# Performance work log

Hardware: AMD Instinct MI355X
Metric: run time of the kernel (lower is better)

## Reference

```python
import jax, jax.numpy as jnp
import numpy as np

WINDOW = 25          # window_size -> h = w = 25, n = 625 tokens
DIM = 512
DIM_HEAD = 64
HEADS = DIM // DIM_HEAD
BATCH = 64


def _rel_pos_indices(ws):
    # mirrors the torch buffer: pairwise relative offsets on a ws x ws grid
    pos = np.arange(ws)
    gi, gj = np.meshgrid(pos, pos, indexing='ij')
    grid = np.stack([gi.reshape(-1), gj.reshape(-1)], axis=-1)      # (ws*ws, 2)
    rel = grid[:, None, :] - grid[None, :, :] + (ws - 1)            # (n, n, 2)
    return (rel[..., 0] * (2 * ws - 1) + rel[..., 1]).astype(np.int32)


def setup_inputs() -> dict:
    key = jax.random.key(0)
    k1, k2, k3, k4 = jax.random.split(key, 4)
    x = jax.random.normal(k1, (BATCH, DIM, WINDOW, WINDOW), jnp.float32)
    w_qkv = jax.random.normal(k2, (DIM, 3 * DIM), jnp.float32) * 0.02   # to_qkv weight (x @ w_qkv)
    w_out = jax.random.normal(k3, (DIM, DIM), jnp.float32) * 0.02       # to_out weight
    rel_pos_bias = jax.random.normal(k4, ((2 * WINDOW - 1) ** 2, HEADS), jnp.float32) * 0.02
    rel_pos_indices = jnp.asarray(_rel_pos_indices(WINDOW))
    return {"x": x, "w_qkv": w_qkv, "w_out": w_out,
            "rel_pos_bias": rel_pos_bias, "rel_pos_indices": rel_pos_indices}


def reference(x, w_qkv, w_out, rel_pos_bias, rel_pos_indices):
    b, d, h, w = x.shape
    n = h * w
    dh = DIM_HEAD
    m = d // dh
    scale = dh ** -0.5
    tokens = x.reshape(b, d, n).transpose(0, 2, 1)                  # b n d
    qkv = tokens @ w_qkv                                            # b n 3d
    q, k, v = jnp.split(qkv, 3, axis=-1)
    split_heads = lambda t: t.reshape(b, n, m, dh).transpose(0, 2, 1, 3)  # b m n dh
    q = split_heads(q) * scale
    k = split_heads(k)
    v = split_heads(v)
    sim = jnp.einsum('bmid,bmjd->bmij', q, k)                       # b m n n
    bias = rel_pos_bias[rel_pos_indices]                            # n n m  (embedding lookup)
    sim = sim + bias.transpose(2, 0, 1)[None]                       # add rel-pos bias inline
    attn = jax.nn.softmax(sim, axis=-1)
    out = jnp.einsum('bmij,bmjd->bmid', attn, v)                    # b m n dh
    out = out.transpose(0, 2, 1, 3).reshape(b, n, m * dh)           # concat heads
    out = out @ w_out                                               # b n d
    return out.transpose(0, 2, 1).reshape(b, d, h, w)
```

## Files before the change

kernel.cpp:

```cpp
#include <hip/hip_runtime.h>
#include <cstdint>
#include <cstddef>

typedef unsigned short u16;
typedef __attribute__((ext_vector_type(8))) short bf16x8;
typedef __attribute__((ext_vector_type(4))) float f32x4;

#define NB    64
#define NTOK  625
#define NTOKP 640
#define DDIM  512
#define NH    8
#define DH    64

__device__ __forceinline__ float bf2f(u16 v) {
    return __uint_as_float(((unsigned int)v) << 16);
}
__device__ __forceinline__ u16 f2bf(float f) {
    unsigned int x = __float_as_uint(f);
    unsigned int r = (x + 0x7fffu + ((x >> 16) & 1u)) >> 16;
    return (u16)r;
}
__device__ __forceinline__ u16 f2bf_fast(float f) {
    return (u16)((__float_as_uint(f) + 0x8000u) >> 16);
}

#if __has_builtin(__builtin_amdgcn_global_load_lds)
#define HAVE_GLDS 1
typedef const __attribute__((address_space(1))) void gas_void;
typedef __attribute__((address_space(3))) void las_void;
__device__ __forceinline__ void glds16(const void* g, void* l) {
    __builtin_amdgcn_global_load_lds((gas_void*)g, (las_void*)l, 16, 0, 0);
}
#else
#define HAVE_GLDS 0
__device__ __forceinline__ void glds16(const void* g, void* l) {
    *(uint4*)l = *(const uint4*)g;
}
#endif

__global__ __launch_bounds__(256) void k_transpose_x(const float* __restrict__ x,
                                                     u16* __restrict__ tokens) {
    __shared__ u16 T[64][66];
    int b = blockIdx.z, ct = blockIdx.y, it = blockIdx.x;
    int t = threadIdx.x;
    int i0 = it * 64, c0 = ct * 64;
#pragma unroll
    for (int r = 0; r < 2; r++) {
        int c = (t >> 3) + r * 32;
        int i8 = (t & 7) * 8;
        const float* s = x + ((size_t)b * DDIM + c0 + c) * NTOK + i0 + i8;
#pragma unroll
        for (int u = 0; u < 8; u++)
            T[c][i8 + u] = (i0 + i8 + u < NTOK) ? f2bf(s[u]) : (u16)0;
    }
    __syncthreads();
#pragma unroll
    for (int r = 0; r < 2; r++) {
        int i = (t >> 3) + r * 32;
        int c8 = (t & 7) * 8;
        int gi = i0 + i;
        if (gi < NTOK) {
            u16* d = tokens + ((size_t)b * NTOK + gi) * DDIM + c0 + c8;
#pragma unroll
            for (int u = 0; u < 8; u++) d[u] = T[c8 + u][i];
        }
    }
}

__global__ __launch_bounds__(256) void k_transpose_w(const float* __restrict__ src,
                                                     u16* __restrict__ dst, int R, int C) {
    __shared__ u16 T[64][66];
    int r0 = blockIdx.y * 64, c0 = blockIdx.x * 64;
    int t = threadIdx.x;
#pragma unroll
    for (int rr = 0; rr < 2; rr++) {
        int r = (t >> 3) + rr * 32;
        int c8 = (t & 7) * 8;
        const float* s = src + (size_t)(r0 + r) * C + c0 + c8;
#pragma unroll
        for (int u = 0; u < 8; u++) T[r][c8 + u] = f2bf(s[u]);
    }
    __syncthreads();
#pragma unroll
    for (int rr = 0; rr < 2; rr++) {
        int c = (t >> 3) + rr * 32;
        int r8 = (t & 7) * 8;
        u16* d = dst + (size_t)(c0 + c) * R + r0 + r8;
#pragma unroll
        for (int u = 0; u < 8; u++) d[u] = T[r8 + u][c];
    }
}

__global__ __launch_bounds__(256) void k_bias(const int* __restrict__ rpi,
                                              const float* __restrict__ rpb,
                                              u16* __restrict__ biasC) {
    int blk = blockIdx.x;
    int m = blk / 100, jt = (blk / 10) % 10, it = blk % 10;
    int t = threadIdx.x;
    u16 vals[16];
#pragma unroll
    for (int jj = 0; jj < 4; jj++) {
        int gj = jt * 64 + jj * 16 + (t & 15);
#pragma unroll
        for (int r = 0; r < 4; r++) {
            int gi = it * 64 + (t >> 6) * 16 + ((t >> 4) & 3) * 4 + r;
            float v;
            if (gj >= NTOK) v = -1e30f;
            else if (gi >= NTOK) v = 0.f;
            else v = rpb[rpi[gi * NTOK + gj] * NH + m];
            vals[jj * 4 + r] = f2bf(v);
        }
    }
    u16* d = biasC + ((size_t)(m * 10 + jt) * 10 + it) * 4096 + t * 16;
    *(uint4*)d = *(uint4*)&vals[0];
    *(uint4*)(d + 8) = *(uint4*)&vals[8];
}

__global__ __launch_bounds__(256) void k_qkv(const u16* __restrict__ tokens,
                                             const u16* __restrict__ wT,
                                             u16* __restrict__ qk, u16* __restrict__ vT) {
    __shared__ u16 SMEM[9216];
    int b = blockIdx.z, jt = blockIdx.y, it = blockIdx.x;
    int i0 = it * 128, j0 = jt * 128;
    int t = threadIdx.x;
    int w = t >> 6, lane = t & 63, quad = lane >> 4, l15 = lane & 15;
    int wr = w >> 1, wc = w & 1;
    f32x4 acc[4][4] = {};
    const u16* abase = tokens + ((size_t)b * NTOK + i0) * DDIM;
    const u16* bbase = wT + (size_t)j0 * DDIM;
    for (int k0 = 0; k0 < DDIM; k0 += 32) {
        __syncthreads();
#pragma unroll
        for (int c = 0; c < 2; c++) {
            int unit = c * 256 + t;
            int row = unit >> 2, col = (unit & 3) * 8;
            glds16(abase + (size_t)row * DDIM + k0 + col, SMEM + unit * 8);
            glds16(bbase + (size_t)row * DDIM + k0 + col, SMEM + 4096 + unit * 8);
        }
        __syncthreads();
        bf16x8 af[4], bfv[4];
#pragma unroll
        for (int q2 = 0; q2 < 4; q2++) {
            af[q2]  = *(const bf16x8*)&SMEM[(wr * 64 + q2 * 16 + l15) * 32 + quad * 8];
            bfv[q2] = *(const bf16x8*)&SMEM[4096 + (wc * 64 + q2 * 16 + l15) * 32 + quad * 8];
        }
#pragma unroll
        for (int ii = 0; ii < 4; ii++)
#pragma unroll
            for (int jj = 0; jj < 4; jj++)
                acc[ii][jj] = __builtin_amdgcn_mfma_f32_16x16x32_bf16(af[ii], bfv[jj], acc[ii][jj], 0, 0, 0);
    }
    __syncthreads();
    if (jt < 8) {
        float scale = (j0 < 512) ? 0.125f : 1.0f;
#pragma unroll
        for (int h = 0; h < 2; h++) {
            if (h) __syncthreads();
            if (wr == h) {
#pragma unroll
                for (int ii = 0; ii < 4; ii++)
#pragma unroll
                    for (int jj = 0; jj < 4; jj++)
#pragma unroll
                        for (int r = 0; r < 4; r++)
                            SMEM[(ii * 16 + quad * 4 + r) * 136 + wc * 64 + jj * 16 + l15] =
                                f2bf(acc[ii][jj][r] * scale);
            }
            __syncthreads();
#pragma unroll
            for (int g = 0; g < 4; g++) {
                int unit = g * 256 + t;
                int tok = unit >> 4, ch8 = (unit & 15) * 8;
                int gi = i0 + h * 64 + tok;
                if (gi < NTOK)
                    *(uint4*)(qk + ((size_t)b * NTOK + gi) * 1024 + j0 + ch8) =
                        *(uint4*)&SMEM[tok * 136 + ch8];
            }
        }
    } else {
        int ch0 = j0 - 1024;
#pragma unroll
        for (int h = 0; h < 2; h++) {
            if (h) __syncthreads();
            if (wr == h) {
#pragma unroll
                for (int ii = 0; ii < 4; ii++)
#pragma unroll
                    for (int jj = 0; jj < 4; jj++)
#pragma unroll
                        for (int r = 0; r < 4; r++) {
                            int tok = ii * 16 + quad * 4 + r;
                            int gi = i0 + h * 64 + tok;
                            u16 val = (gi < NTOK) ? f2bf(acc[ii][jj][r]) : (u16)0;
                            SMEM[(wc * 64 + jj * 16 + l15) * 72 + (tok & 15) * 4 + (tok >> 4)] = val;
                        }
            }
            __syncthreads();
#pragma unroll
            for (int g = 0; g < 4; g++) {
                int unit = g * 256 + t;
                int chl = unit >> 3, tok8 = (unit & 7) * 8;
                int chv = ch0 + chl, hd = chv >> 6, tc = chv & 63;
                *(uint4*)(vT + (((size_t)b * NH + hd) * DH + tc) * NTOKP + i0 + h * 64 + tok8) =
                    *(uint4*)&SMEM[chl * 72 + tok8];
            }
        }
    }
}

__global__ __launch_bounds__(256) void k_attn(const u16* __restrict__ qk,
                                              const u16* __restrict__ vT,
                                              const u16* __restrict__ biasC,
                                              u16* __restrict__ attnout) {
    __shared__ u16 Qs[64][72];
    __shared__ u16 Ks[64][72];
    __shared__ u16 Vs[64][72];
    __shared__ u16 Ps[64][72];
    int b = blockIdx.z, m = blockIdx.y, it = blockIdx.x;
    int i0 = it * 64;
    int t = threadIdx.x;
    int w = t >> 6, lane = t & 63, quad = lane >> 4, l15 = lane & 15;
#pragma unroll
    for (int r = 0; r < 2; r++) {
        int row = (t >> 3) + r * 32;
        int t8 = (t & 7) * 8;
        int gi = i0 + row;
        uint4 v;
        if (gi < NTOK) v = *(const uint4*)(qk + ((size_t)b * NTOK + gi) * 1024 + m * DH + t8);
        else v = make_uint4(0, 0, 0, 0);
        *(uint4*)&Qs[row][t8] = v;
    }
    float rs[4] = {0.f, 0.f, 0.f, 0.f};
    f32x4 oacc[4] = {};
    const u16* vbase = vT + ((size_t)b * NH + m) * DH * NTOKP;
    const u16* bC = biasC + (size_t)(m * 10) * 10 * 4096 + (size_t)it * 4096 + t * 16;

    for (int jt = 0; jt < 10; jt++) {
        int j0 = jt * 64;
        __syncthreads();
#pragma unroll
        for (int r = 0; r < 2; r++) {
            int row = (t >> 3) + r * 32;
            int c8 = (t & 7) * 8;
            int gj = j0 + row;
            uint4 kv;
            if (gj < NTOK) kv = *(const uint4*)(qk + ((size_t)b * NTOK + gj) * 1024 + 512 + m * DH + c8);
            else kv = make_uint4(0, 0, 0, 0);
            *(uint4*)&Ks[row][c8] = kv;
            uint4 vv = *(const uint4*)(vbase + (size_t)row * NTOKP + j0 + c8);
            *(uint4*)&Vs[row][c8] = vv;
        }
        __syncthreads();
        const u16* bp = bC + (size_t)jt * 10 * 4096;
        uint4 bb0 = *(const uint4*)bp, bb1 = *(const uint4*)(bp + 8);
        u16 bh[16];
        *(uint4*)&bh[0] = bb0; *(uint4*)&bh[8] = bb1;
        f32x4 s[4];
#pragma unroll
        for (int jj = 0; jj < 4; jj++)
#pragma unroll
            for (int r = 0; r < 4; r++) s[jj][r] = bf2f(bh[jj * 4 + r]);
        bf16x8 aq[2];
#pragma unroll
        for (int kk = 0; kk < 2; kk++)
            aq[kk] = *(const bf16x8*)&Qs[w * 16 + l15][kk * 32 + quad * 8];
#pragma unroll
        for (int jj = 0; jj < 4; jj++)
#pragma unroll
            for (int kk = 0; kk < 2; kk++) {
                bf16x8 bk = *(const bf16x8*)&Ks[jj * 16 + l15][kk * 32 + quad * 8];
                s[jj] = __builtin_amdgcn_mfma_f32_16x16x32_bf16(aq[kk], bk, s[jj], 0, 0, 0);
            }
#pragma unroll
        for (int r = 0; r < 4; r++) {
            float p0 = __expf(s[0][r]), p1 = __expf(s[1][r]);
            float p2 = __expf(s[2][r]), p3 = __expf(s[3][r]);
            rs[r] += (p0 + p1) + (p2 + p3);
            uint2 pk;
            pk.x = (unsigned)f2bf_fast(p0) | ((unsigned)f2bf_fast(p1) << 16);
            pk.y = (unsigned)f2bf_fast(p2) | ((unsigned)f2bf_fast(p3) << 16);
            *(uint2*)&Ps[w * 16 + quad * 4 + r][l15 * 4] = pk;
        }
        bf16x8 ap[2];
#pragma unroll
        for (int kk = 0; kk < 2; kk++)
            ap[kk] = *(const bf16x8*)&Ps[w * 16 + l15][kk * 32 + quad * 8];
#pragma unroll
        for (int tt = 0; tt < 4; tt++)
#pragma unroll
            for (int kk = 0; kk < 2; kk++) {
                bf16x8 bv = *(const bf16x8*)&Vs[tt * 16 + l15][kk * 32 + quad * 8];
                oacc[tt] = __builtin_amdgcn_mfma_f32_16x16x32_bf16(ap[kk], bv, oacc[tt], 0, 0, 0);
            }
    }
    float rinv[4];
#pragma unroll
    for (int r = 0; r < 4; r++) {
        float sum = rs[r];
#pragma unroll
        for (int d = 1; d < 16; d <<= 1) sum += __shfl_xor(sum, d, 64);
        rinv[r] = __frcp_rn(sum);
    }
#pragma unroll
    for (int tt = 0; tt < 4; tt++)
#pragma unroll
        for (int r = 0; r < 4; r++) {
            int gi = i0 + w * 16 + quad * 4 + r;
            if (gi < NTOK)
                attnout[((size_t)b * NTOK + gi) * DDIM + m * DH + tt * 16 + l15] =
                    f2bf(oacc[tt][r] * rinv[r]);
        }
}

__global__ __launch_bounds__(256) void k_out(const u16* __restrict__ attnout,
                                             const u16* __restrict__ woT,
                                             float* __restrict__ out) {
    __shared__ u16 SMEM[8192];
    int b = blockIdx.z, jt = blockIdx.y, it = blockIdx.x;
    int j0 = jt * 128, i0 = it * 128;
    int t = threadIdx.x;
    int w = t >> 6, lane = t & 63, quad = lane >> 4, l15 = lane & 15;
    int wr = w >> 1, wc = w & 1;
    f32x4 acc[4][4] = {};
    const u16* abase = woT + (size_t)j0 * DDIM;
    const u16* bbase = attnout + ((size_t)b * NTOK + i0) * DDIM;
    for (int k0 = 0; k0 < DDIM; k0 += 32) {
        __syncthreads();
#pragma unroll
        for (int c = 0; c < 2; c++) {
            int unit = c * 256 + t;
            int row = unit >> 2, col = (unit & 3) * 8;
            glds16(abase + (size_t)row * DDIM + k0 + col, SMEM + unit * 8);
            glds16(bbase + (size_t)row * DDIM + k0 + col, SMEM + 4096 + unit * 8);
        }
        __syncthreads();
        bf16x8 af[4], bfv[4];
#pragma unroll
        for (int q2 = 0; q2 < 4; q2++) {
            af[q2]  = *(const bf16x8*)&SMEM[(wr * 64 + q2 * 16 + l15) * 32 + quad * 8];
            bfv[q2] = *(const bf16x8*)&SMEM[4096 + (wc * 64 + q2 * 16 + l15) * 32 + quad * 8];
        }
#pragma unroll
        for (int ii = 0; ii < 4; ii++)
#pragma unroll
            for (int jj = 0; jj < 4; jj++)
                acc[ii][jj] = __builtin_amdgcn_mfma_f32_16x16x32_bf16(af[ii], bfv[jj], acc[ii][jj], 0, 0, 0);
    }
#pragma unroll
    for (int ii = 0; ii < 4; ii++)
#pragma unroll
        for (int jj = 0; jj < 4; jj++) {
            int gi = i0 + wc * 64 + jj * 16 + l15;
            if (gi >= NTOK) continue;
#pragma unroll
            for (int r = 0; r < 4; r++) {
                int gj = j0 + wr * 64 + ii * 16 + quad * 4 + r;
                out[((size_t)b * DDIM + gj) * NTOK + gi] = acc[ii][jj][r];
            }
        }
}

extern "C" void kernel_launch(void* const* d_in, const int* in_sizes, int n_in,
                              void* d_out, int out_size, void* d_ws, size_t ws_size,
                              hipStream_t stream) {
    const float* x    = (const float*)d_in[0];
    const float* wqkv = (const float*)d_in[1];
    const float* wout = (const float*)d_in[2];
    const float* rpb  = (const float*)d_in[3];
    const int*   rpi  = (const int*)d_in[4];
    float* out = (float*)d_out;

    char* ws = (char*)d_ws;
    size_t off = 0;
    auto alloc = [&](size_t nbytes) -> void* {
        void* p = ws + off;
        off += (nbytes + 255) & ~(size_t)255;
        return p;
    };
    u16* tokens   = (u16*)alloc((size_t)NB * NTOK * DDIM * 2);
    u16* qk       = (u16*)alloc((size_t)NB * NTOK * 1024 * 2);
    u16* vT       = (u16*)alloc((size_t)NB * NH * DH * NTOKP * 2);
    u16* wqkvT    = (u16*)alloc((size_t)1536 * DDIM * 2);
    u16* woutT    = (u16*)alloc((size_t)DDIM * DDIM * 2);
    u16* biasC    = (u16*)alloc((size_t)NH * 100 * 4096 * 2);
    u16* attnout  = tokens;

    k_transpose_x<<<dim3(10, 8, NB), 256, 0, stream>>>(x, tokens);
    k_transpose_w<<<dim3(1536 / 64, DDIM / 64), 256, 0, stream>>>(wqkv, wqkvT, DDIM, 1536);
    k_transpose_w<<<dim3(DDIM / 64, DDIM / 64), 256, 0, stream>>>(wout, woutT, DDIM, DDIM);
    k_bias<<<dim3(800), 256, 0, stream>>>(rpi, rpb, biasC);
    k_qkv<<<dim3(5, 12, NB), 256, 0, stream>>>(tokens, wqkvT, qk, vT);
    k_attn<<<dim3(10, NH, NB), 256, 0, stream>>>(qk, vT, biasC, attnout);
    k_out<<<dim3(5, 4, NB), 256, 0, stream>>>(attnout, woutT, out);
}
```

Measured before the change: 487.8 us.

## Swizzle GEMM LDS tiles with K=64, remap block ids, fold softmax rowsum into MFMA

The QKV and output GEMMs now stage K=64 per iteration in an XOR-swizzled LDS layout to halve barriers and avoid bank conflicts. Block indices are flattened and remapped so groups of 8 consecutive blocks, which the hardware typically spreads across XCDs, share weight/head data. The attention kernel computes the softmax denominator by appending a row of ones to V as an extra MFMA tile, removing per-row shuffle reductions. The bias table is stored as fp32, removing bf16 unpacking but doubling bias read traffic.

Measured after the change: 508.8 us. 1.04x slower.

```diff
diff --git a/kernel.cpp b/kernel.cpp
--- a/kernel.cpp
+++ b/kernel.cpp
@@ -26,14 +26,12 @@
 }
 
 #if __has_builtin(__builtin_amdgcn_global_load_lds)
-#define HAVE_GLDS 1
 typedef const __attribute__((address_space(1))) void gas_void;
 typedef __attribute__((address_space(3))) void las_void;
 __device__ __forceinline__ void glds16(const void* g, void* l) {
     __builtin_amdgcn_global_load_lds((gas_void*)g, (las_void*)l, 16, 0, 0);
 }
 #else
-#define HAVE_GLDS 0
 __device__ __forceinline__ void glds16(const void* g, void* l) {
     *(uint4*)l = *(const uint4*)g;
 }
@@ -94,11 +92,11 @@
 
 __global__ __launch_bounds__(256) void k_bias(const int* __restrict__ rpi,
                                               const float* __restrict__ rpb,
-                                              u16* __restrict__ biasC) {
+                                              float* __restrict__ biasCf) {
     int blk = blockIdx.x;
     int m = blk / 100, jt = (blk / 10) % 10, it = blk % 10;
     int t = threadIdx.x;
-    u16 vals[16];
+    float vals[16];
 #pragma unroll
     for (int jj = 0; jj < 4; jj++) {
         int gj = jt * 64 + jj * 16 + (t & 15);
@@ -109,19 +107,24 @@
             if (gj >= NTOK) v = -1e30f;
             else if (gi >= NTOK) v = 0.f;
             else v = rpb[rpi[gi * NTOK + gj] * NH + m];
-            vals[jj * 4 + r] = f2bf(v);
-        }
-    }
-    u16* d = biasC + ((size_t)(m * 10 + jt) * 10 + it) * 4096 + t * 16;
-    *(uint4*)d = *(uint4*)&vals[0];
-    *(uint4*)(d + 8) = *(uint4*)&vals[8];
+            vals[jj * 4 + r] = v;
+        }
+    }
+    float* d = biasCf + ((size_t)(m * 10 + jt) * 10 + it) * 4096 + t * 16;
+#pragma unroll
+    for (int g = 0; g < 4; g++)
+        *(f32x4*)(d + g * 4) = *(f32x4*)&vals[g * 4];
 }
 
 __global__ __launch_bounds__(256) void k_qkv(const u16* __restrict__ tokens,
                                              const u16* __restrict__ wT,
                                              u16* __restrict__ qk, u16* __restrict__ vT) {
-    __shared__ u16 SMEM[9216];
-    int b = blockIdx.z, jt = blockIdx.y, it = blockIdx.x;
+    __shared__ u16 SMEM[16384];
+    int bid = blockIdx.x;
+    int c8id = bid & 7, t2 = bid >> 3;
+    int jt = t2 % 12, q_ = t2 / 12;
+    int itb = q_ * 8 + c8id;
+    int it = itb % 5, b = itb / 5;
     int i0 = it * 128, j0 = jt * 128;
     int t = threadIdx.x;
     int w = t >> 6, lane = t & 63, quad = lane >> 4, l15 = lane & 15;
@@ -129,27 +132,32 @@
     f32x4 acc[4][4] = {};
     const u16* abase = tokens + ((size_t)b * NTOK + i0) * DDIM;
     const u16* bbase = wT + (size_t)j0 * DDIM;
-    for (int k0 = 0; k0 < DDIM; k0 += 32) {
-        __syncthreads();
-#pragma unroll
-        for (int c = 0; c < 2; c++) {
+    for (int k0 = 0; k0 < DDIM; k0 += 64) {
+        __syncthreads();
+#pragma unroll
+        for (int c = 0; c < 4; c++) {
             int unit = c * 256 + t;
-            int row = unit >> 2, col = (unit & 3) * 8;
-            glds16(abase + (size_t)row * DDIM + k0 + col, SMEM + unit * 8);
-            glds16(bbase + (size_t)row * DDIM + k0 + col, SMEM + 4096 + unit * 8);
-        }
-        __syncthreads();
-        bf16x8 af[4], bfv[4];
-#pragma unroll
-        for (int q2 = 0; q2 < 4; q2++) {
-            af[q2]  = *(const bf16x8*)&SMEM[(wr * 64 + q2 * 16 + l15) * 32 + quad * 8];
-            bfv[q2] = *(const bf16x8*)&SMEM[4096 + (wc * 64 + q2 * 16 + l15) * 32 + quad * 8];
-        }
-#pragma unroll
-        for (int ii = 0; ii < 4; ii++)
-#pragma unroll
-            for (int jj = 0; jj < 4; jj++)
-                acc[ii][jj] = __builtin_amdgcn_mfma_f32_16x16x32_bf16(af[ii], bfv[jj], acc[ii][jj], 0, 0, 0);
+            int row = unit >> 3, cc = unit & 7;
+            int gcol = (cc ^ (row & 7)) * 8;
+            glds16(abase + (size_t)row * DDIM + k0 + gcol, SMEM + unit * 8);
+            glds16(bbase + (size_t)row * DDIM + k0 + gcol, SMEM + 8192 + unit * 8);
+        }
+        __syncthreads();
+#pragma unroll
+        for (int kk = 0; kk < 2; kk++) {
+            bf16x8 af[4], bfv[4];
+            int chA = (((kk * 4 + quad) ^ (l15 & 7))) * 8;
+#pragma unroll
+            for (int q2 = 0; q2 < 4; q2++) {
+                af[q2]  = *(const bf16x8*)&SMEM[(wr * 64 + q2 * 16 + l15) * 64 + chA];
+                bfv[q2] = *(const bf16x8*)&SMEM[8192 + (wc * 64 + q2 * 16 + l15) * 64 + chA];
+            }
+#pragma unroll
+            for (int ii = 0; ii < 4; ii++)
+#pragma unroll
+                for (int jj = 0; jj < 4; jj++)
+                    acc[ii][jj] = __builtin_amdgcn_mfma_f32_16x16x32_bf16(af[ii], bfv[jj], acc[ii][jj], 0, 0, 0);
+        }
     }
     __syncthreads();
     if (jt < 8) {
@@ -211,16 +219,24 @@
 
 __global__ __launch_bounds__(256) void k_attn(const u16* __restrict__ qk,
                                               const u16* __restrict__ vT,
-                                              const u16* __restrict__ biasC,
+                                              const float* __restrict__ biasCf,
                                               u16* __restrict__ attnout) {
     __shared__ u16 Qs[64][72];
     __shared__ u16 Ks[64][72];
-    __shared__ u16 Vs[64][72];
+    __shared__ u16 Vs[80][72];
     __shared__ u16 Ps[64][72];
-    int b = blockIdx.z, m = blockIdx.y, it = blockIdx.x;
+    int bid = blockIdx.x;
+    int c8id = bid & 7, t2 = bid >> 3;
+    int it = t2 % 10, q_ = t2 / 10;
+    int bm = q_ * 8 + c8id;
+    int m = bm & 7, b = bm >> 3;
     int i0 = it * 64;
     int t = threadIdx.x;
     int w = t >> 6, lane = t & 63, quad = lane >> 4, l15 = lane & 15;
+    {
+        int row = 64 + (t >> 4), c4 = (t & 15) * 4;
+        *(uint2*)&Vs[row][c4] = make_uint2(0x3F803F80u, 0x3F803F80u);
+    }
 #pragma unroll
     for (int r = 0; r < 2; r++) {
         int row = (t >> 3) + r * 32;
@@ -231,10 +247,9 @@
         else v = make_uint4(0, 0, 0, 0);
         *(uint4*)&Qs[row][t8] = v;
     }
-    float rs[4] = {0.f, 0.f, 0.f, 0.f};
-    f32x4 oacc[4] = {};
+    f32x4 oacc[5] = {};
     const u16* vbase = vT + ((size_t)b * NH + m) * DH * NTOKP;
-    const u16* bC = biasC + (size_t)(m * 10) * 10 * 4096 + (size_t)it * 4096 + t * 16;
+    const float* bC = biasCf + (size_t)(m * 100 + it) * 4096 + t * 16;
 
     for (int jt = 0; jt < 10; jt++) {
         int j0 = jt * 64;
@@ -252,15 +267,10 @@
             *(uint4*)&Vs[row][c8] = vv;
         }
         __syncthreads();
-        const u16* bp = bC + (size_t)jt * 10 * 4096;
-        uint4 bb0 = *(const uint4*)bp, bb1 = *(const uint4*)(bp + 8);
-        u16 bh[16];
-        *(uint4*)&bh[0] = bb0; *(uint4*)&bh[8] = bb1;
+        const float* bp = bC + (size_t)jt * 10 * 4096;
         f32x4 s[4];
 #pragma unroll
-        for (int jj = 0; jj < 4; jj++)
-#pragma unroll
-            for (int r = 0; r < 4; r++) s[jj][r] = bf2f(bh[jj * 4 + r]);
+        for (int jj = 0; jj < 4; jj++) s[jj] = *(const f32x4*)(bp + jj * 4);
         bf16x8 aq[2];
 #pragma unroll
         for (int kk = 0; kk < 2; kk++)
@@ -276,7 +286,6 @@
         for (int r = 0; r < 4; r++) {
             float p0 = __expf(s[0][r]), p1 = __expf(s[1][r]);
             float p2 = __expf(s[2][r]), p3 = __expf(s[3][r]);
-            rs[r] += (p0 + p1) + (p2 + p3);
             uint2 pk;
             pk.x = (unsigned)f2bf_fast(p0) | ((unsigned)f2bf_fast(p1) << 16);
             pk.y = (unsigned)f2bf_fast(p2) | ((unsigned)f2bf_fast(p3) << 16);
@@ -287,7 +296,7 @@
         for (int kk = 0; kk < 2; kk++)
             ap[kk] = *(const bf16x8*)&Ps[w * 16 + l15][kk * 32 + quad * 8];
 #pragma unroll
-        for (int tt = 0; tt < 4; tt++)
+        for (int tt = 0; tt < 5; tt++)
 #pragma unroll
             for (int kk = 0; kk < 2; kk++) {
                 bf16x8 bv = *(const bf16x8*)&Vs[tt * 16 + l15][kk * 32 + quad * 8];
@@ -296,12 +305,7 @@
     }
     float rinv[4];
 #pragma unroll
-    for (int r = 0; r < 4; r++) {
-        float sum = rs[r];
-#pragma unroll
-        for (int d = 1; d < 16; d <<= 1) sum += __shfl_xor(sum, d, 64);
-        rinv[r] = __frcp_rn(sum);
-    }
+    for (int r = 0; r < 4; r++) rinv[r] = __frcp_rn(oacc[4][r]);
 #pragma unroll
     for (int tt = 0; tt < 4; tt++)
 #pragma unroll
@@ -316,8 +320,12 @@
 __global__ __launch_bounds__(256) void k_out(const u16* __restrict__ attnout,
                                              const u16* __restrict__ woT,
                                              float* __restrict__ out) {
-    __shared__ u16 SMEM[8192];
-    int b = blockIdx.z, jt = blockIdx.y, it = blockIdx.x;
+    __shared__ u16 SMEM[16384];
+    int bid = blockIdx.x;
+    int c8id = bid & 7, t2 = bid >> 3;
+    int jt = t2 % 4, q_ = t2 / 4;
+    int itb = q_ * 8 + c8id;
+    int it = itb % 5, b = itb / 5;
     int j0 = jt * 128, i0 = it * 128;
     int t = threadIdx.x;
     int w = t >> 6, lane = t & 63, quad = lane >> 4, l15 = lane & 15;
@@ -325,27 +333,32 @@
     f32x4 acc[4][4] = {};
     const u16* abase = woT + (size_t)j0 * DDIM;
     const u16* bbase = attnout + ((size_t)b * NTOK + i0) * DDIM;
-    for (int k0 = 0; k0 < DDIM; k0 += 32) {
-        __syncthreads();
-#pragma unroll
-        for (int c = 0; c < 2; c++) {
+    for (int k0 = 0; k0 < DDIM; k0 += 64) {
+        __syncthreads();
+#pragma unroll
+        for (int c = 0; c < 4; c++) {
             int unit = c * 256 + t;
-            int row = unit >> 2, col = (unit & 3) * 8;
-            glds16(abase + (size_t)row * DDIM + k0 + col, SMEM + unit * 8);
-            glds16(bbase + (size_t)row * DDIM + k0 + col, SMEM + 4096 + unit * 8);
-        }
-        __syncthreads();
-        bf16x8 af[4], bfv[4];
-#pragma unroll
-        for (int q2 = 0; q2 < 4; q2++) {
-            af[q2]  = *(const bf16x8*)&SMEM[(wr * 64 + q2 * 16 + l15) * 32 + quad * 8];
-            bfv[q2] = *(const bf16x8*)&SMEM[4096 + (wc * 64 + q2 * 16 + l15) * 32 + quad * 8];
-        }
-#pragma unroll
-        for (int ii = 0; ii < 4; ii++)
-#pragma unroll
-            for (int jj = 0; jj < 4; jj++)
-                acc[ii][jj] = __builtin_amdgcn_mfma_f32_16x16x32_bf16(af[ii], bfv[jj], acc[ii][jj], 0, 0, 0);
+            int row = unit >> 3, cc = unit & 7;
+            int gcol = (cc ^ (row & 7)) * 8;
+            glds16(abase + (size_t)row * DDIM + k0 + gcol, SMEM + unit * 8);
+            glds16(bbase + (size_t)row * DDIM + k0 + gcol, SMEM + 8192 + unit * 8);
+        }
+        __syncthreads();
+#pragma unroll
+        for (int kk = 0; kk < 2; kk++) {
+            bf16x8 af[4], bfv[4];
+            int chA = (((kk * 4 + quad) ^ (l15 & 7))) * 8;
+#pragma unroll
+            for (int q2 = 0; q2 < 4; q2++) {
+                af[q2]  = *(const bf16x8*)&SMEM[(wr * 64 + q2 * 16 + l15) * 64 + chA];
+                bfv[q2] = *(const bf16x8*)&SMEM[8192 + (wc * 64 + q2 * 16 + l15) * 64 + chA];
+            }
+#pragma unroll
+            for (int ii = 0; ii < 4; ii++)
+#pragma unroll
+                for (int jj = 0; jj < 4; jj++)
+                    acc[ii][jj] = __builtin_amdgcn_mfma_f32_16x16x32_bf16(af[ii], bfv[jj], acc[ii][jj], 0, 0, 0);
+        }
     }
 #pragma unroll
     for (int ii = 0; ii < 4; ii++)
@@ -383,14 +396,14 @@
     u16* vT       = (u16*)alloc((size_t)NB * NH * DH * NTOKP * 2);
     u16* wqkvT    = (u16*)alloc((size_t)1536 * DDIM * 2);
     u16* woutT    = (u16*)alloc((size_t)DDIM * DDIM * 2);
-    u16* biasC    = (u16*)alloc((size_t)NH * 100 * 4096 * 2);
+    float* biasCf = (float*)alloc((size_t)NH * 100 * 4096 * 4);
     u16* attnout  = tokens;
 
     k_transpose_x<<<dim3(10, 8, NB), 256, 0, stream>>>(x, tokens);
     k_transpose_w<<<dim3(1536 / 64, DDIM / 64), 256, 0, stream>>>(wqkv, wqkvT, DDIM, 1536);
     k_transpose_w<<<dim3(DDIM / 64, DDIM / 64), 256, 0, stream>>>(wout, woutT, DDIM, DDIM);
-    k_bias<<<dim3(800), 256, 0, stream>>>(rpi, rpb, biasC);
-    k_qkv<<<dim3(5, 12, NB), 256, 0, stream>>>(tokens, wqkvT, qk, vT);
-    k_attn<<<dim3(10, NH, NB), 256, 0, stream>>>(qk, vT, biasC, attnout);
-    k_out<<<dim3(5, 4, NB), 256, 0, stream>>>(attnout, woutT, out);
-}
+    k_bias<<<dim3(800), 256, 0, stream>>>(rpi, rpb, biasCf);
+    k_qkv<<<dim3(3840), 256, 0, stream>>>(tokens, wqkvT, qk, vT);
+    k_attn<<<dim3(5120), 256, 0, stream>>>(qk, vT, biasCf, attnout);
+    k_out<<<dim3(1280), 256, 0, stream>>>(attnout, woutT, out);
+}
```
